# Kernel optimization log

Hardware: AMD Instinct MI355X
Metric: run time of the kernel (lower is better)

## Reference

```python
import jax, jax.numpy as jnp
import numpy as np

V, E, D, FN, FE, G = 20000, 100000, 32, 36, 12, 1000
DEPTH, S2S_ITERS = 3, 6


def setup_inputs() -> dict:
    key = jax.random.key(0)
    ks = jax.random.split(key, 30)
    rn = lambda k, s, sc=0.1: (jax.random.normal(k, s, jnp.float32) * sc)
    inp = {
        "node": jax.random.normal(ks[0], (V, FN), jnp.float32),
        "edge": jax.random.normal(ks[1], (E, FE), jnp.float32),
        "src": jax.random.randint(ks[2], (V,) if False else (E,), 0, V, jnp.int32),
        "dst": jax.random.randint(ks[3], (E,), 0, V, jnp.int32),
        "node2graph": jnp.sort(jax.random.randint(ks[4], (V,), 0, G, jnp.int32)),
        # embeddings
        "Wn": rn(ks[5], (FN, D)), "bn": jnp.zeros((D,), jnp.float32),
        "We": rn(ks[6], (FE, D)), "be": jnp.zeros((D,), jnp.float32),
        # per-layer edge network (stacked over depth)
        "eW1": rn(ks[7], (DEPTH, D, 2 * D)), "eb1": jnp.zeros((DEPTH, 2 * D), jnp.float32),
        "eW2": rn(ks[8], (DEPTH, 2 * D, D * D), 0.02), "eb2": jnp.zeros((DEPTH, D * D), jnp.float32),
        # per-layer GRUCell (torch layout: [3D, in])
        "gru_wih": rn(ks[9], (DEPTH, 3 * D, D)), "gru_whh": rn(ks[10], (DEPTH, 3 * D, D)),
        "gru_bih": jnp.zeros((DEPTH, 3 * D), jnp.float32), "gru_bhh": jnp.zeros((DEPTH, 3 * D), jnp.float32),
        # per-layer LayerNorm
        "ln_g": jnp.ones((DEPTH, D), jnp.float32), "ln_b": jnp.zeros((DEPTH, D), jnp.float32),
        # Set2Set LSTMCell: input 2D -> hidden D (torch gate order i,f,g,o)
        "lstm_wih": rn(ks[11], (4 * D, 2 * D)), "lstm_whh": rn(ks[12], (4 * D, D)),
        "lstm_bih": jnp.zeros((4 * D,), jnp.float32), "lstm_bhh": jnp.zeros((4 * D,), jnp.float32),
        # prediction MLP
        "Wp1": rn(ks[13], (2 * D, D)), "bp1": jnp.zeros((D,), jnp.float32),
        "Wp2": rn(ks[14], (D, 1)), "bp2": jnp.zeros((1,), jnp.float32),
    }
    return inp


def _leaky(x):
    return jnp.where(x > 0, x, 0.01 * x)


def _forward(node, edge, src, dst, node2graph, Wn, bn, We, be, eW1, eb1, eW2, eb2,
             gru_wih, gru_whh, gru_bih, gru_bhh, ln_g, ln_b,
             lstm_wih, lstm_whh, lstm_bih, lstm_bhh, Wp1, bp1, Wp2, bp2):
    h = _leaky(node @ Wn + bn)            # (V, D) embedded nodes
    e_h = _leaky(edge @ We + be)          # (E, D) embedded edges
    hidden0 = h                           # GRU hidden is the initial embedding (never updated in source)
    for l in range(DEPTH):
        # edge-conditioned weights: (E, D, D)
        ew = jax.nn.relu(e_h @ eW1[l] + eb1[l]) @ eW2[l] + eb2[l]
        Wmat = ew.reshape(E, D, D)
        msg = jnp.einsum('ed,edf->ef', h[src], Wmat)          # gather + per-edge matmul
        agg = jax.ops.segment_sum(msg, dst, num_segments=V)   # scatter-sum to dst nodes
        agg = jax.nn.relu(agg)
        # torch GRUCell(agg, hidden0)
        gi = agg @ gru_wih[l].T + gru_bih[l]
        gh = hidden0 @ gru_whh[l].T + gru_bhh[l]
        ir, iz, inn = jnp.split(gi, 3, axis=-1)
        hr, hz, hn = jnp.split(gh, 3, axis=-1)
        r = jax.nn.sigmoid(ir + hr)
        z = jax.nn.sigmoid(iz + hz)
        n = jnp.tanh(inn + r * hn)
        hnew = (1.0 - z) * n + z * hidden0
        # LayerNorm
        mu = hnew.mean(-1, keepdims=True)
        var = ((hnew - mu) ** 2).mean(-1, keepdims=True)
        h = (hnew - mu) * jax.lax.rsqrt(var + 1e-5) * ln_g[l] + ln_b[l]
    # Set2Set readout over graphs
    q_star = jnp.zeros((G, 2 * D), jnp.float32)
    hh = jnp.zeros((G, D), jnp.float32)
    cc = jnp.zeros((G, D), jnp.float32)
    for _ in range(S2S_ITERS):
        gates = q_star @ lstm_wih.T + lstm_bih + hh @ lstm_whh.T + lstm_bhh
        i, f, g, o = jnp.split(gates, 4, axis=-1)
        cc = jax.nn.sigmoid(f) * cc + jax.nn.sigmoid(i) * jnp.tanh(g)
        hh = jax.nn.sigmoid(o) * jnp.tanh(cc)
        q = hh                                                 # (G, D)
        att = jnp.sum(h * q[node2graph], axis=-1)              # (V,)
        m = jax.ops.segment_max(att, node2graph, num_segments=G)
        ex = jnp.exp(att - m[node2graph])
        denom = jax.ops.segment_sum(ex, node2graph, num_segments=G)
        alpha = ex / denom[node2graph]
        r_read = jax.ops.segment_sum(alpha[:, None] * h, node2graph, num_segments=G)
        q_star = jnp.concatenate([q, r_read], axis=-1)
    out = jax.nn.relu(q_star @ Wp1 + bp1) @ Wp2 + bp2          # (G, 1)
    return out


def reference(node, edge, src, dst, node2graph, Wn, bn, We, be, eW1, eb1, eW2, eb2,
              gru_wih, gru_whh, gru_bih, gru_bhh, ln_g, ln_b,
              lstm_wih, lstm_whh, lstm_bih, lstm_bhh, Wp1, bp1, Wp2, bp2):
    return _forward(node, edge, src, dst, node2graph, Wn, bn, We, be, eW1, eb1, eW2, eb2,
                    gru_wih, gru_whh, gru_bih, gru_bhh, ln_g, ln_b,
                    lstm_wih, lstm_whh, lstm_bih, lstm_bhh, Wp1, bp1, Wp2, bp2)
```

## Files before the change

### kernel.cpp

```cpp
#include <hip/hip_runtime.h>
#include <math.h>

#define NV 20000
#define NE 100000
#define DD 32
#define NG 1000
#define NDEPTH 3
#define S2S 6
#define NBK 8
#define EPB 16
#define CAPN 128
#define SCAN_T 256
#define SCAN_C 80

__device__ __forceinline__ float sigmoidf_(float x) { return 1.0f / (1.0f + __expf(-x)); }

__global__ void k_prolog(const float* __restrict__ node, const float* __restrict__ Wn,
                         const float* __restrict__ bn, float* __restrict__ h,
                         float* __restrict__ h0,
                         const float* __restrict__ edge, const float* __restrict__ We,
                         const float* __restrict__ be, float* __restrict__ e_h,
                         const int* __restrict__ n2g, int* __restrict__ gstart,
                         int* __restrict__ deg) {
    __shared__ float sWn[36 * DD];
    __shared__ float sbn[DD];
    __shared__ float sxn[32][36];
    __shared__ float sWe[12 * DD];
    __shared__ float sbe[DD];
    __shared__ float sxe[32][12];
    int tid = threadIdx.x;
    int b = blockIdx.x;
    if (b < 625) {
        for (int i = tid; i < 36 * DD; i += 256) sWn[i] = Wn[i];
        if (tid < DD) sbn[tid] = bn[tid];
        int v0 = b * 32;
        for (int i = tid; i < 32 * 36; i += 256) sxn[i / 36][i % 36] = node[(size_t)v0 * 36 + i];
        __syncthreads();
        int f = tid & 31;
        int nb = tid >> 5;
        for (int g = 0; g < 4; ++g) {
            int n = nb + 8 * g;
            float acc = sbn[f];
            #pragma unroll
            for (int i = 0; i < 36; ++i) acc += sxn[n][i] * sWn[i * DD + f];
            float y = acc > 0.f ? acc : 0.01f * acc;
            h[(size_t)(v0 + n) * DD + f] = y;
            h0[(size_t)(v0 + n) * DD + f] = y;
        }
    } else if (b < 3750) {
        for (int i = tid; i < 12 * DD; i += 256) sWe[i] = We[i];
        if (tid < DD) sbe[tid] = be[tid];
        int e0 = (b - 625) * 32;
        for (int i = tid; i < 32 * 12; i += 256) sxe[i / 12][i % 12] = edge[(size_t)e0 * 12 + i];
        __syncthreads();
        int f = tid & 31;
        int nb = tid >> 5;
        for (int g = 0; g < 4; ++g) {
            int n = nb + 8 * g;
            float acc = sbe[f];
            #pragma unroll
            for (int i = 0; i < 12; ++i) acc += sxe[n][i] * sWe[i * DD + f];
            float y = acc > 0.f ? acc : 0.01f * acc;
            e_h[(size_t)(e0 + n) * DD + f] = y;
        }
    } else if (b < 3755) {
        int g = (b - 3750) * 256 + tid;
        if (g <= NG) {
            int lo = 0, hi = NV;
            while (lo < hi) {
                int mid = (lo + hi) >> 1;
                if (n2g[mid] < g) lo = mid + 1; else hi = mid;
            }
            gstart[g] = lo;
        }
    } else {
        int i = (b - 3755) * 256 + tid;
        if (i < NV) deg[i] = 0;
    }
}

__global__ void k_scan(const int* __restrict__ deg, int* __restrict__ estart, int* __restrict__ cur) {
    __shared__ int sdeg[SCAN_T * SCAN_C];
    __shared__ int spart[SCAN_T];
    int tid = threadIdx.x;
    for (int i = tid; i < SCAN_T * SCAN_C; i += SCAN_T) sdeg[i] = (i < NV) ? deg[i] : 0;
    __syncthreads();
    int base = tid * SCAN_C;
    int sum = 0;
    for (int j = 0; j < SCAN_C; ++j) sum += sdeg[base + j];
    spart[tid] = sum;
    __syncthreads();
    for (int off = 1; off < SCAN_T; off <<= 1) {
        int v = (tid >= off) ? spart[tid - off] : 0;
        __syncthreads();
        spart[tid] += v;
        __syncthreads();
    }
    int run = spart[tid] - sum;
    for (int j = 0; j < SCAN_C; ++j) {
        int idx = base + j;
        if (idx < NV) { estart[idx] = run; cur[idx] = run; }
        run += sdeg[base + j];
    }
    if (tid == SCAN_T - 1) estart[NV] = run;
}

__global__ void k_scatter(const int* __restrict__ src, int* __restrict__ cur,
                          int* __restrict__ esorted) {
    int e = blockIdx.x * blockDim.x + threadIdx.x;
    if (e < NE) {
        int s = src[e];
        int pos = atomicAdd(&cur[s], 1);
        esorted[pos] = e;
    }
}

__global__ void k_edge_t3(const float* __restrict__ e_h, const float* __restrict__ eW1,
                          const float* __restrict__ eb1, float* __restrict__ t3,
                          float* __restrict__ agg,
                          const int* __restrict__ src, int* __restrict__ deg) {
    __shared__ float sW[DD * 64];
    __shared__ float sb[64];
    int tid = threadIdx.x;
    int b = blockIdx.x;
    if (b >= NDEPTH * (NE / EPB)) {
        int e = (b - NDEPTH * (NE / EPB)) * 256 + tid;
        if (e < NE) atomicAdd(&deg[src[e]], 1);
        return;
    }
    if (b < (NV * DD) / 256) agg[(size_t)b * 256 + tid] = 0.f;
    int l = b / (NE / EPB), bb = b % (NE / EPB);
    const float* W = eW1 + (size_t)l * DD * 64;
    float* t = t3 + (size_t)l * NE * 64;
    for (int i = tid; i < DD * 64; i += 256) sW[i] = W[i];
    if (tid < 64) sb[tid] = eb1[l * 64 + tid];
    int e0 = bb * EPB;
    __syncthreads();
    int k = tid & 63;
    int nb = tid >> 6;
    float acc[4];
    #pragma unroll
    for (int g = 0; g < 4; ++g) acc[g] = sb[k];
    #pragma unroll
    for (int d4 = 0; d4 < 8; ++d4) {
        float4 ex[4];
        #pragma unroll
        for (int g = 0; g < 4; ++g)
            ex[g] = *(const float4*)(e_h + (size_t)(e0 + nb + 4 * g) * DD + d4 * 4);
        #pragma unroll
        for (int dd = 0; dd < 4; ++dd) {
            float w = sW[(d4 * 4 + dd) * 64 + k];
            #pragma unroll
            for (int g = 0; g < 4; ++g)
                acc[g] = fmaf((&ex[g].x)[dd], w, acc[g]);
        }
    }
    #pragma unroll
    for (int g = 0; g < 4; ++g)
        t[(size_t)(e0 + nb + 4 * g) * 64 + k] = fmaxf(acc[g], 0.f);
}

__global__ __launch_bounds__(1024, 8) void k_fused(const float* __restrict__ h,
        const float* __restrict__ eW2, const float* __restrict__ eb2,
        const float* __restrict__ t, const int* __restrict__ dst,
        const int* __restrict__ estart, const int* __restrict__ esorted,
        float* __restrict__ agg) {
    int v0 = blockIdx.x * NBK;
    __shared__ float sA[NBK][64][32];
    __shared__ float sbb[NBK][32];
    int tid = threadIdx.x;
    int lane = tid & 63;

    float4 hv4 = *(const float4*)(h + (size_t)(v0 + (lane >> 3)) * DD + 4 * (lane & 7));
    float ha[4] = {hv4.x, hv4.y, hv4.z, hv4.w};

    int f = tid & 31;
    int kb = tid >> 5;
    const float* wbase = eW2 + kb * 1024 + f;

    float acc[2][8];
    #pragma unroll
    for (int jj = 0; jj < 2; ++jj)
        #pragma unroll
        for (int n = 0; n < 8; ++n) acc[jj][n] = 0.f;

    #pragma unroll
    for (int d4 = 0; d4 < 8; ++d4) {
        float hs[8][4];
        #pragma unroll
        for (int n = 0; n < 8; ++n)
            #pragma unroll
            for (int dd = 0; dd < 4; ++dd)
                hs[n][dd] = __builtin_bit_cast(float,
                    __builtin_amdgcn_readlane(__builtin_bit_cast(int, ha[dd]), n * 8 + d4));
        #pragma unroll
        for (int jj = 0; jj < 2; ++jj) {
            const float* wp = wbase + jj * 32 * 1024 + d4 * 4 * 32;
            #pragma unroll
            for (int dd = 0; dd < 4; ++dd) {
                float w = wp[dd * 32];
                #pragma unroll
                for (int n = 0; n < 8; ++n) acc[jj][n] = fmaf(hs[n][dd], w, acc[jj][n]);
            }
        }
    }
    #pragma unroll
    for (int jj = 0; jj < 2; ++jj)
        #pragma unroll
        for (int n = 0; n < 8; ++n)
            sA[n][kb + 32 * jj][f] = acc[jj][n];

    if (tid < 256) {
        int n = tid >> 5;
        float bacc = 0.f;
        #pragma unroll
        for (int d = 0; d < DD; ++d) {
            float hvv = __shfl(ha[d & 3], n * 8 + (d >> 2), 64);
            bacc = fmaf(hvv, eb2[d * 32 + f], bacc);
        }
        sbb[n][f] = bacc;
    }
    __syncthreads();

    int w = tid >> 6;
    int n = w >> 1;
    int par = w & 1;
    int hf = lane >> 5;
    float Areg[32];
    #pragma unroll
    for (int q = 0; q < 32; ++q)
        Areg[q] = sA[n][2 * q + hf][f];
    float bbv = sbb[n][f];
    int i = estart[v0 + n] + par, e1 = estart[v0 + n + 1];
    if (i < e1) {
        int e = esorted[i];
        float tv = t[(size_t)e * 64 + lane];
        int dn = dst[e];
        while (i < e1) {
            i += 2;
            float tv2 = 0.f; int dn2 = 0;
            if (i < e1) {
                int e2 = esorted[i];
                tv2 = t[(size_t)e2 * 64 + lane];
                dn2 = dst[e2];
            }
            float m0 = 0.f, m1 = 0.f, m2 = 0.f, m3 = 0.f;
            #pragma unroll
            for (int q = 0; q < 32; q += 4) {
                m0 = fmaf(__shfl(tv, 2 * q + hf, 64),       Areg[q],     m0);
                m1 = fmaf(__shfl(tv, 2 * (q + 1) + hf, 64), Areg[q + 1], m1);
                m2 = fmaf(__shfl(tv, 2 * (q + 2) + hf, 64), Areg[q + 2], m2);
                m3 = fmaf(__shfl(tv, 2 * (q + 3) + hf, 64), Areg[q + 3], m3);
            }
            float m = (m0 + m1) + (m2 + m3);
            m += __shfl_xor(m, 32, 64);
            if (lane < 32) atomicAdd(&agg[(size_t)dn * DD + f], m + bbv);
            tv = tv2; dn = dn2;
        }
    }
}

__global__ __launch_bounds__(256, 2) void k_gru_ln(float* __restrict__ agg,
                         const float* __restrict__ h0,
                         const float* __restrict__ wih, const float* __restrict__ whh,
                         const float* __restrict__ bih, const float* __restrict__ bhh,
                         const float* __restrict__ lng, const float* __restrict__ lnb,
                         float* __restrict__ h) {
    __shared__ float sWT[2][3][32][33];
    __shared__ float sbih[96], sbhh[96], sg[DD], sb[DD];
    int tid = threadIdx.x;
    for (int i = tid; i < 3072; i += 256) {
        int g = i >> 10, j = (i >> 5) & 31, f = i & 31;
        sWT[0][g][f][j] = wih[i];
        sWT[1][g][f][j] = whh[i];
    }
    if (tid < 96) { sbih[tid] = bih[tid]; sbhh[tid] = bhh[tid]; }
    if (tid < DD) { sg[tid] = lng[tid]; sb[tid] = lnb[tid]; }
    int v0 = blockIdx.x * 8;
    __syncthreads();
    int j = tid & 31;
    int n = v0 + (tid >> 5);
    float4 aq[8], hq[8];
    #pragma unroll
    for (int f4 = 0; f4 < 8; ++f4) {
        float4 a = *(const float4*)(agg + (size_t)n * DD + f4 * 4);
        a.x = fmaxf(a.x, 0.f); a.y = fmaxf(a.y, 0.f); a.z = fmaxf(a.z, 0.f); a.w = fmaxf(a.w, 0.f);
        aq[f4] = a;
        hq[f4] = *(const float4*)(h0 + (size_t)n * DD + f4 * 4);
    }
    agg[(size_t)n * DD + j] = 0.f;
    float h0j = h0[(size_t)n * DD + j];
    float gi0 = 0.f, gi1 = 0.f, gi2 = 0.f, gh0 = 0.f, gh1 = 0.f, gh2 = 0.f;
    #pragma unroll
    for (int f4 = 0; f4 < 8; ++f4) {
        #pragma unroll
        for (int dd = 0; dd < 4; ++dd) {
            int f = f4 * 4 + dd;
            float a = (&aq[f4].x)[dd], hh = (&hq[f4].x)[dd];
            gi0 = fmaf(a, sWT[0][0][f][j], gi0);
            gi1 = fmaf(a, sWT[0][1][f][j], gi1);
            gi2 = fmaf(a, sWT[0][2][f][j], gi2);
            gh0 = fmaf(hh, sWT[1][0][f][j], gh0);
            gh1 = fmaf(hh, sWT[1][1][f][j], gh1);
            gh2 = fmaf(hh, sWT[1][2][f][j], gh2);
        }
    }
    float r = sigmoidf_(gi0 + sbih[j] + gh0 + sbhh[j]);
    float z = sigmoidf_(gi1 + sbih[DD + j] + gh1 + sbhh[DD + j]);
    float nn = tanhf(gi2 + sbih[2 * DD + j] + r * (gh2 + sbhh[2 * DD + j]));
    float hnew = (1.f - z) * nn + z * h0j;
    float mu = hnew;
    #pragma unroll
    for (int o = 16; o; o >>= 1) mu += __shfl_xor(mu, o, 64);
    mu *= (1.f / DD);
    float d = hnew - mu;
    float var = d * d;
    #pragma unroll
    for (int o = 16; o; o >>= 1) var += __shfl_xor(var, o, 64);
    var *= (1.f / DD);
    float inv = rsqrtf(var + 1e-5f);
    h[(size_t)n * DD + j] = d * inv * sg[j] + sb[j];
}

__global__ __launch_bounds__(256) void k_s2s(const float* __restrict__ h,
                      const int* __restrict__ gstart,
                      const float* __restrict__ wih, const float* __restrict__ whh,
                      const float* __restrict__ bih, const float* __restrict__ bhh,
                      const float* __restrict__ Wp1, const float* __restrict__ bp1,
                      const float* __restrict__ Wp2, const float* __restrict__ bp2,
                      float* __restrict__ attbuf, float* __restrict__ out) {
    int g = blockIdx.x, tid = threadIdx.x;
    int s = gstart[g], e = gstart[g + 1], cnt = e - s;
    bool inlds = (cnt <= CAPN);
    __shared__ float sh[CAPN * 33];
    __shared__ float qs[64], shh[32], scc[32], gbuf[128];
    __shared__ float satt[256];
    __shared__ float red[4];
    __shared__ float rpart[8][32];
    if (inlds) {
        for (int idx = tid; idx < cnt * 32; idx += 256) {
            int v = idx >> 5, f = idx & 31;
            sh[v * 33 + f] = h[(size_t)(s + v) * 32 + f];
        }
    }
    if (tid < 64) qs[tid] = 0.f;
    if (tid < 32) { shh[tid] = 0.f; scc[tid] = 0.f; }
    __syncthreads();
    for (int it = 0; it < S2S; ++it) {
        if (tid < 128) {
            float gv = bih[tid] + bhh[tid];
            const float4* w4 = (const float4*)(wih + tid * 64);
            #pragma unroll
            for (int i = 0; i < 16; ++i) {
                float4 w = w4[i];
                gv += qs[4 * i] * w.x + qs[4 * i + 1] * w.y + qs[4 * i + 2] * w.z + qs[4 * i + 3] * w.w;
            }
            const float4* u4 = (const float4*)(whh + tid * 32);
            #pragma unroll
            for (int i = 0; i < 8; ++i) {
                float4 w = u4[i];
                gv += shh[4 * i] * w.x + shh[4 * i + 1] * w.y + shh[4 * i + 2] * w.z + shh[4 * i + 3] * w.w;
            }
            gbuf[tid] = gv;
        }
        __syncthreads();
        if (tid < 32) {
            float ii = gbuf[tid], ff = gbuf[32 + tid], gg = gbuf[64 + tid], oo = gbuf[96 + tid];
            float c = sigmoidf_(ff) * scc[tid] + sigmoidf_(ii) * tanhf(gg);
            scc[tid] = c;
            float hv = sigmoidf_(oo) * tanhf(c);
            shh[tid] = hv;
            qs[tid] = hv;
        }
        __syncthreads();
        float pmax = -1e30f;
        if (inlds) {
            float a = -1e30f;
            if (tid < cnt) {
                float acc = 0.f;
                #pragma unroll
                for (int f = 0; f < 32; ++f) acc += sh[tid * 33 + f] * shh[f];
                a = acc;
            }
            satt[tid] = a;
            pmax = a;
        } else {
            for (int v = tid; v < cnt; v += 256) {
                float acc = 0.f;
                const float* hp = h + (size_t)(s + v) * 32;
                #pragma unroll
                for (int f = 0; f < 32; ++f) acc += hp[f] * shh[f];
                attbuf[s + v] = acc;
                pmax = fmaxf(pmax, acc);
            }
        }
        #pragma unroll
        for (int o = 32; o; o >>= 1) pmax = fmaxf(pmax, __shfl_xor(pmax, o, 64));
        if ((tid & 63) == 0) red[tid >> 6] = pmax;
        __syncthreads();
        float m = fmaxf(fmaxf(red[0], red[1]), fmaxf(red[2], red[3]));
        float psum = 0.f;
        if (inlds) {
            if (tid < cnt) { float exv = __expf(satt[tid] - m); satt[tid] = exv; psum = exv; }
        } else {
            for (int v = tid; v < cnt; v += 256) {
                float exv = __expf(attbuf[s + v] - m); attbuf[s + v] = exv; psum += exv;
            }
        }
        #pragma unroll
        for (int o = 32; o; o >>= 1) psum += __shfl_xor(psum, o, 64);
        __syncthreads();
        if ((tid & 63) == 0) red[tid >> 6] = psum;
        __syncthreads();
        float denom = red[0] + red[1] + red[2] + red[3];
        int f = tid & 31, vc = tid >> 5;
        float racc = 0.f;
        if (inlds) {
            for (int v = vc; v < cnt; v += 8) racc += satt[v] * sh[v * 33 + f];
        } else {
            for (int v = vc; v < cnt; v += 8) racc += attbuf[s + v] * h[(size_t)(s + v) * 32 + f];
        }
        rpart[vc][f] = racc;
        __syncthreads();
        if (tid < 32) {
            float r = 0.f;
            #pragma unroll
            for (int c2 = 0; c2 < 8; ++c2) r += rpart[c2][tid];
            qs[32 + tid] = (cnt > 0) ? (r / denom) : 0.f;
        }
        __syncthreads();
    }
    if (tid < 32) {
        float u = bp1[tid];
        #pragma unroll
        for (int p = 0; p < 64; ++p) u += qs[p] * Wp1[p * 32 + tid];
        u = fmaxf(u, 0.f);
        float pr = u * Wp2[tid];
        #pragma unroll
        for (int o = 16; o; o >>= 1) pr += __shfl_xor(pr, o, 64);
        if (tid == 0) out[g] = pr + bp2[0];
    }
}

extern "C" void kernel_launch(void* const* d_in, const int* in_sizes, int n_in,
                              void* d_out, int out_size, void* d_ws, size_t ws_size,
                              hipStream_t stream) {
    const float* node = (const float*)d_in[0];
    const float* edge = (const float*)d_in[1];
    const int*   src  = (const int*)d_in[2];
    const int*   dst  = (const int*)d_in[3];
    const int*   n2g  = (const int*)d_in[4];
    const float* Wn   = (const float*)d_in[5];
    const float* bn   = (const float*)d_in[6];
    const float* We   = (const float*)d_in[7];
    const float* be   = (const float*)d_in[8];
    const float* eW1  = (const float*)d_in[9];
    const float* eb1  = (const float*)d_in[10];
    const float* eW2  = (const float*)d_in[11];
    const float* eb2  = (const float*)d_in[12];
    const float* gwih = (const float*)d_in[13];
    const float* gwhh = (const float*)d_in[14];
    const float* gbih = (const float*)d_in[15];
    const float* gbhh = (const float*)d_in[16];
    const float* lng  = (const float*)d_in[17];
    const float* lnb  = (const float*)d_in[18];
    const float* lwih = (const float*)d_in[19];
    const float* lwhh = (const float*)d_in[20];
    const float* lbih = (const float*)d_in[21];
    const float* lbhh = (const float*)d_in[22];
    const float* Wp1  = (const float*)d_in[23];
    const float* bp1  = (const float*)d_in[24];
    const float* Wp2  = (const float*)d_in[25];
    const float* bp2  = (const float*)d_in[26];

    float* ws = (float*)d_ws;
    float* h    = ws; ws += (size_t)NV * DD;
    float* h0   = ws; ws += (size_t)NV * DD;
    float* e_h  = ws; ws += (size_t)NE * DD;
    float* t3   = ws; ws += (size_t)NE * 64 * NDEPTH;
    float* agg  = ws; ws += (size_t)NV * DD;
    float* attbuf = ws; ws += NV;
    int* deg     = (int*)ws; ws += NV;
    int* cur     = (int*)ws; ws += NV;
    int* estart  = (int*)ws; ws += (NV + 1);
    int* esorted = (int*)ws; ws += NE;
    int* gstart  = (int*)ws; ws += (NG + 1);

    k_prolog<<<3755 + (NV + 255) / 256, 256, 0, stream>>>(node, Wn, bn, h, h0,
                                                          edge, We, be, e_h,
                                                          n2g, gstart, deg);
    k_edge_t3<<<NDEPTH * (NE / EPB) + (NE + 255) / 256, 256, 0, stream>>>(
        e_h, eW1, eb1, t3, agg, src, deg);
    k_scan<<<1, SCAN_T, 0, stream>>>(deg, estart, cur);
    k_scatter<<<(NE + 255) / 256, 256, 0, stream>>>(src, cur, esorted);

    for (int l = 0; l < NDEPTH; ++l) {
        k_fused<<<NV / NBK, 1024, 0, stream>>>(h, eW2 + (size_t)l * 64 * 1024, eb2 + l * 1024,
                                               t3 + (size_t)l * NE * 64, dst, estart, esorted, agg);
        k_gru_ln<<<NV / 8, 256, 0, stream>>>(agg, h0,
                                             gwih + (size_t)l * 96 * DD, gwhh + (size_t)l * 96 * DD,
                                             gbih + l * 96, gbhh + l * 96,
                                             lng + l * DD, lnb + l * DD, h);
    }

    k_s2s<<<NG, 256, 0, stream>>>(h, gstart, lwih, lwhh, lbih, lbhh, Wp1, bp1, Wp2, bp2,
                                  attbuf, (float*)d_out);
}
```

Measured before the change: 567.8 us.

## Balance per-block edge work across waves and double edges per block in t3 kernel

The fused message kernel no longer assigns two waves to each of its 8 nodes. All 16 waves now split the block's whole contiguous edge range evenly. The local node index is packed into the upper bits of the sorted edge ids so each wave can reload its A-matrix registers from shared memory when the source node changes. This aims to remove load imbalance from skewed node degrees, at the cost of occasional register reloads. Separately, the edge-MLP kernel processes 32 edges per block instead of 16, which halves the number of weight loads into shared memory.

Result: faster. 519.9 us (-8.4%).

```diff
diff --git a/kernel.cpp b/kernel.cpp
--- a/kernel.cpp
+++ b/kernel.cpp
@@ -8,7 +8,7 @@
 #define NDEPTH 3
 #define S2S 6
 #define NBK 8
-#define EPB 16
+#define EPB 32
 #define CAPN 128
 #define SCAN_T 256
 #define SCAN_C 80
@@ -111,7 +111,7 @@
     if (e < NE) {
         int s = src[e];
         int pos = atomicAdd(&cur[s], 1);
-        esorted[pos] = e;
+        esorted[pos] = e | ((s & (NBK - 1)) << 28);
     }
 }
 
@@ -138,25 +138,25 @@
     __syncthreads();
     int k = tid & 63;
     int nb = tid >> 6;
-    float acc[4];
-    #pragma unroll
-    for (int g = 0; g < 4; ++g) acc[g] = sb[k];
+    float acc[8];
+    #pragma unroll
+    for (int g = 0; g < 8; ++g) acc[g] = sb[k];
     #pragma unroll
     for (int d4 = 0; d4 < 8; ++d4) {
-        float4 ex[4];
-        #pragma unroll
-        for (int g = 0; g < 4; ++g)
+        float4 ex[8];
+        #pragma unroll
+        for (int g = 0; g < 8; ++g)
             ex[g] = *(const float4*)(e_h + (size_t)(e0 + nb + 4 * g) * DD + d4 * 4);
         #pragma unroll
         for (int dd = 0; dd < 4; ++dd) {
             float w = sW[(d4 * 4 + dd) * 64 + k];
             #pragma unroll
-            for (int g = 0; g < 4; ++g)
+            for (int g = 0; g < 8; ++g)
                 acc[g] = fmaf((&ex[g].x)[dd], w, acc[g]);
         }
     }
     #pragma unroll
-    for (int g = 0; g < 4; ++g)
+    for (int g = 0; g < 8; ++g)
         t[(size_t)(e0 + nb + 4 * g) * 64 + k] = fmaxf(acc[g], 0.f);
 }
 
@@ -223,26 +223,36 @@
     __syncthreads();
 
     int w = tid >> 6;
-    int n = w >> 1;
-    int par = w & 1;
     int hf = lane >> 5;
+    int e0b = estart[v0], e1b = estart[v0 + NBK];
+    int total = e1b - e0b;
+    int chunk = (total + 15) >> 4;
+    int is = e0b + w * chunk;
+    int ie = is + chunk; if (ie > e1b) ie = e1b;
     float Areg[32];
-    #pragma unroll
-    for (int q = 0; q < 32; ++q)
-        Areg[q] = sA[n][2 * q + hf][f];
-    float bbv = sbb[n][f];
-    int i = estart[v0 + n] + par, e1 = estart[v0 + n + 1];
-    if (i < e1) {
-        int e = esorted[i];
+    float bbv = 0.f;
+    int curn = -1;
+    if (is < ie) {
+        int pk = esorted[is];
+        int e = pk & 0xFFFFFF, ls = pk >> 28;
         float tv = t[(size_t)e * 64 + lane];
         int dn = dst[e];
-        while (i < e1) {
-            i += 2;
-            float tv2 = 0.f; int dn2 = 0;
-            if (i < e1) {
-                int e2 = esorted[i];
+        int i = is;
+        while (i < ie) {
+            ++i;
+            float tv2 = 0.f; int dn2 = 0, ls2 = 0;
+            if (i < ie) {
+                int pk2 = esorted[i];
+                int e2 = pk2 & 0xFFFFFF; ls2 = pk2 >> 28;
                 tv2 = t[(size_t)e2 * 64 + lane];
                 dn2 = dst[e2];
+            }
+            if (ls != curn) {
+                curn = ls;
+                #pragma unroll
+                for (int q = 0; q < 32; ++q)
+                    Areg[q] = sA[ls][2 * q + hf][f];
+                bbv = sbb[ls][f];
             }
             float m0 = 0.f, m1 = 0.f, m2 = 0.f, m3 = 0.f;
             #pragma unroll
@@ -255,7 +265,7 @@
             float m = (m0 + m1) + (m2 + m3);
             m += __shfl_xor(m, 32, 64);
             if (lane < 32) atomicAdd(&agg[(size_t)dn * DD + f], m + bbv);
-            tv = tv2; dn = dn2;
+            tv = tv2; dn = dn2; ls = ls2;
         }
     }
 }
```
